# Kernel optimization log

Measured on AMD Instinct MI355X. Metric: run time of the kernel, lower is better.

## Reference

```python
import jax, jax.numpy as jnp
import numpy as np

WIN = 7      # window_size (square)
HEADS = 6    # num_heads


def setup_inputs() -> dict:
    key = jax.random.key(0)
    k0, k1, k2, k3 = jax.random.split(key, 4)
    B, C, H, W = 8, 384, 56, 56
    x = jax.random.normal(k0, (B, C, H, W), jnp.float32)
    # 1x1 conv weights stored as (out, in) matrices
    w_qkv = jax.random.normal(k1, (3 * C, C), jnp.float32) * 0.02
    b_qkv = jnp.zeros((3 * C,), jnp.float32)
    w_proj = jax.random.normal(k2, (C, C), jnp.float32) * 0.02
    b_proj = jnp.zeros((C,), jnp.float32)
    bias_table = jax.random.normal(k3, (WIN * WIN, HEADS), jnp.float32) * 0.02
    return {"x": x, "w_qkv": w_qkv, "b_qkv": b_qkv, "w_proj": w_proj,
            "b_proj": b_proj, "bias_table": bias_table}


def reference(x, w_qkv, b_qkv, w_proj, b_proj, bias_table):
    B, C, H, W = x.shape
    heads, win = HEADS, WIN
    dph = C // heads
    scale = dph ** -0.5
    # qkv 1x1 conv -> (B, 3C, H, W)
    qkv = jnp.einsum('bcij,oc->boij', x, w_qkv) + b_qkv[None, :, None, None]
    q = qkv[:, :C] * scale
    k = qkv[:, C:2 * C]
    v = qkv[:, 2 * C:]
    p = win // 2
    kp = jnp.pad(k, ((0, 0), (0, 0), (p, p), (p, p)))  # (B,C,H+6,W+6)
    vp = jnp.pad(v, ((0, 0), (0, 0), (p, p), (p, p)))
    qh = q.reshape(B, heads, dph, H, W)
    # local window QK scores: fixed 49 shifted slices (no big patch tensor)
    scores = []
    for idx in range(win * win):
        dy, dx = idx // win, idx % win
        ks = kp[:, :, dy:dy + H, dx:dx + W].reshape(B, heads, dph, H, W)
        scores.append(jnp.einsum('bhdij,bhdij->bhij', qh, ks))
    attn = jnp.stack(scores, axis=2)  # (B, heads, 49, H, W)
    # forward() adds relative_position_bias * 0 (faithful no-op)
    attn = attn + bias_table.T.reshape(1, heads, win * win, 1, 1) * 0.0
    attn = jax.nn.softmax(attn, axis=2)
    # apply attention to V via the same 49 shifted slices
    out = jnp.zeros((B, heads, dph, H, W), x.dtype)
    for idx in range(win * win):
        dy, dx = idx // win, idx % win
        vs = vp[:, :, dy:dy + H, dx:dx + W].reshape(B, heads, dph, H, W)
        out = out + attn[:, :, idx][:, :, None] * vs
    out = out.reshape(B, C, H, W)
    # proj 1x1 conv; proj_drop has p=0.0 -> identity
    out = jnp.einsum('bcij,oc->boij', out, w_proj) + b_proj[None, :, None, None]
    return out
```

## Files before the change

kernel.cpp:

```cpp
#include <hip/hip_runtime.h>
#include <hip/hip_bf16.h>
#include <stdint.h>

#define HWsz 3136
#define Hh   56
#define Cc   384
#define NHEADS 6
#define NB   8

typedef __attribute__((ext_vector_type(8))) short short8;
typedef __attribute__((ext_vector_type(4))) short short4v;
typedef __attribute__((ext_vector_type(4))) float f32x4;

static __device__ __forceinline__ short f2bf(float f) {
  __hip_bfloat16 h = __float2bfloat16(f);
  return (short)__builtin_bit_cast(unsigned short, h);
}

__global__ void prep_weights(const float* __restrict__ wq, const float* __restrict__ wp,
                             short* __restrict__ wqb, short* __restrict__ wpb) {
  int stride = gridDim.x * blockDim.x;
  for (int i = blockIdx.x * blockDim.x + threadIdx.x; i < 3 * Cc * Cc; i += stride) {
    float v = wq[i];
    if (i < Cc * Cc) v *= 0.125f;
    wqb[i] = f2bf(v);
  }
  for (int i = blockIdx.x * blockDim.x + threadIdx.x; i < Cc * Cc; i += stride)
    wpb[i] = f2bf(wp[i]);
}

__global__ __launch_bounds__(256) void transpose_x(const float* __restrict__ x, short* __restrict__ xT) {
  __shared__ float tile[32][33];
  int b = blockIdx.z;
  int p0 = blockIdx.x * 32, c0 = blockIdx.y * 32;
  int t = threadIdx.x;
  const float* xb = x + (size_t)b * Cc * HWsz;
  int tp = t & 31, tc = t >> 5;
#pragma unroll
  for (int cc = 0; cc < 4; ++cc)
    tile[tc + cc * 8][tp] = xb[(size_t)(c0 + tc + cc * 8) * HWsz + p0 + tp];
  __syncthreads();
  short* xo = xT + (size_t)b * HWsz * Cc;
  int wc = t & 31, wp = t >> 5;
#pragma unroll
  for (int pp = 0; pp < 4; ++pp)
    xo[(size_t)(p0 + wp + pp * 8) * Cc + c0 + wc] = f2bf(tile[wc][wp + pp * 8]);
}

template<int MODE>
__global__ __launch_bounds__(256) void gemm_bf16(
    const short* __restrict__ A, const short* __restrict__ Bm,
    const float* __restrict__ bias, void* __restrict__ o1, void* __restrict__ o2)
{
  constexpr int K = Cc;
  const int b   = blockIdx.z;
  const int om0 = blockIdx.x * 128;
  const int pn0 = blockIdx.y * 128;
  __shared__ short lA[128 * 40];
  __shared__ short lB[128 * 40];
  const int t    = threadIdx.x;
  const int lane = t & 63;
  const int wave = t >> 6;
  const int wm = (wave >> 1) * 64;
  const int wn = (wave & 1) * 64;
  f32x4 acc[4][4] = {};
  const short* Bb = Bm + (size_t)b * HWsz * K;
  const int sr = t >> 2;
  const int sk = (t & 3) * 8;
  int pr0 = pn0 + sr;      if (pr0 > HWsz - 1) pr0 = HWsz - 1;
  int pr1 = pn0 + sr + 64; if (pr1 > HWsz - 1) pr1 = HWsz - 1;
  const int fr = lane & 15;
  const int fo = lane >> 4;
  for (int k0 = 0; k0 < K; k0 += 32) {
    short8 a0 = *(const short8*)(A + (size_t)(om0 + sr) * K + k0 + sk);
    short8 a1 = *(const short8*)(A + (size_t)(om0 + sr + 64) * K + k0 + sk);
    short8 b0 = *(const short8*)(Bb + (size_t)pr0 * K + k0 + sk);
    short8 b1 = *(const short8*)(Bb + (size_t)pr1 * K + k0 + sk);
    __syncthreads();
    *(short8*)(lA + sr * 40 + sk) = a0;
    *(short8*)(lA + (sr + 64) * 40 + sk) = a1;
    *(short8*)(lB + sr * 40 + sk) = b0;
    *(short8*)(lB + (sr + 64) * 40 + sk) = b1;
    __syncthreads();
    short8 af[4], bfr[4];
#pragma unroll
    for (int m = 0; m < 4; ++m) af[m]  = *(const short8*)(lA + (wm + m * 16 + fr) * 40 + fo * 8);
#pragma unroll
    for (int n = 0; n < 4; ++n) bfr[n] = *(const short8*)(lB + (wn + n * 16 + fr) * 40 + fo * 8);
#pragma unroll
    for (int m = 0; m < 4; ++m)
#pragma unroll
      for (int n = 0; n < 4; ++n)
        acc[m][n] = __builtin_amdgcn_mfma_f32_16x16x32_bf16(af[m], bfr[n], acc[m][n], 0, 0, 0);
  }
  if (MODE == 0) {
    if (om0 < 768) {
      short* outq = (short*)o1 + (size_t)b * HWsz * 768;
#pragma unroll
      for (int m = 0; m < 4; ++m) {
        int ob = om0 + wm + m * 16 + (lane >> 4) * 4;
        float bs[4];
#pragma unroll
        for (int r = 0; r < 4; ++r) { int o = ob + r; bs[r] = bias[o] * (o < Cc ? 0.125f : 1.0f); }
#pragma unroll
        for (int n = 0; n < 4; ++n) {
          int p = pn0 + wn + n * 16 + fr;
          if (p < HWsz) {
            short4v s;
#pragma unroll
            for (int r = 0; r < 4; ++r) s[r] = f2bf(acc[m][n][r] + bs[r]);
            *(short4v*)(outq + (size_t)p * 768 + ob) = s;
          }
        }
      }
    } else {
      short* vtp = (short*)o2;
#pragma unroll
      for (int m = 0; m < 4; ++m) {
        int ob = om0 + wm + m * 16 + (lane >> 4) * 4;
#pragma unroll
        for (int n = 0; n < 4; ++n) {
          int p = pn0 + wn + n * 16 + fr;
          if (p < HWsz) {
            int ii = p / Hh, jj = p % Hh;
#pragma unroll
            for (int r = 0; r < 4; ++r) {
              int ch = ob + r - 768;
              vtp[((b * Cc + ch) * 62 + ii + 3) * 64 + jj + 3] = f2bf(acc[m][n][r] + bias[ob + r]);
            }
          }
        }
      }
    }
  } else {
    float* outo = (float*)o1 + (size_t)b * Cc * HWsz;
#pragma unroll
    for (int m = 0; m < 4; ++m) {
      int ob = om0 + wm + m * 16 + (lane >> 4) * 4;
#pragma unroll
      for (int n = 0; n < 4; ++n) {
        int p = pn0 + wn + n * 16 + fr;
        if (p < HWsz) {
#pragma unroll
          for (int r = 0; r < 4; ++r)
            outo[(size_t)(ob + r) * HWsz + p] = acc[m][n][r] + bias[ob + r];
        }
      }
    }
  }
}

__global__ __launch_bounds__(256) void attn_mfma(
    const short* __restrict__ qkv,
    const short* __restrict__ vtp,
    short* __restrict__ aout)
{
  __shared__ short P[64 * 40];
  const int bh = blockIdx.z;
  const int b = bh / NHEADS, h = bh % NHEADS;
  const int i0 = blockIdx.y * 8, j0 = blockIdx.x * 8;
  const int t = threadIdx.x, lane = t & 63, w = t >> 6;
  const int fr = lane & 15, fo = lane >> 4;

  const int q_idx = w * 16 + fr;
  const int qr = q_idx >> 3, qc = q_idx & 7;
  const int qkvb = b * HWsz * 768;

  const short* qp = qkv + qkvb + ((i0 + qr) * Hh + j0 + qc) * 768 + h * 64 + fo * 8;
  short8 qf0 = *(const short8*)(qp);
  short8 qf1 = *(const short8*)(qp + 32);

  const int kj = j0 + fr - 3;
  const bool jok = (unsigned)kj < (unsigned)Hh;
  const int kjs = kj < 0 ? 0 : (kj > Hh - 1 ? Hh - 1 : kj);
  const short* kcol = qkv + qkvb + Cc + h * 64 + fo * 8;

  const short8 z = (short8)0;
  f32x4 oacc[4] = {};
  float sum = 0.f;

#pragma unroll 2
  for (int kc = 0; kc < 7; ++kc) {
    short8 kf[2][2];
#pragma unroll
    for (int mloc = 0; mloc < 2; ++mloc) {
      int ki = i0 + 2 * kc + mloc - 3;
      bool ok = jok && ((unsigned)ki < (unsigned)Hh);
      int kis = ki < 0 ? 0 : (ki > Hh - 1 ? Hh - 1 : ki);
      const short8* ka = (const short8*)(kcol + (kis * Hh + kjs) * 768);
      short8 k0 = ka[0], k1 = ka[4];
      kf[mloc][0] = ok ? k0 : z;
      kf[mloc][1] = ok ? k1 : z;
    }
    short8 vf[4];
    const int vrow = i0 + 2 * kc + (fo >> 1);
    const int vcol = j0 + (fo & 1) * 8;
#pragma unroll
    for (int n = 0; n < 4; ++n)
      vf[n] = *(const short8*)(vtp + ((b * Cc + h * 64 + 16 * n + fr) * 62 + vrow) * 64 + vcol);
    f32x4 s0 = {}, s1 = {};
    s0 = __builtin_amdgcn_mfma_f32_16x16x32_bf16(kf[0][0], qf0, s0, 0, 0, 0);
    s0 = __builtin_amdgcn_mfma_f32_16x16x32_bf16(kf[0][1], qf1, s0, 0, 0, 0);
    s1 = __builtin_amdgcn_mfma_f32_16x16x32_bf16(kf[1][0], qf0, s1, 0, 0, 0);
    s1 = __builtin_amdgcn_mfma_f32_16x16x32_bf16(kf[1][1], qf1, s1, 0, 0, 0);
#pragma unroll
    for (int mloc = 0; mloc < 2; ++mloc) {
      const f32x4 sv = mloc ? s1 : s0;
      int dpr = 2 * kc + mloc - qr;
      bool rok = (unsigned)dpr <= 6u;
      short4v pk;
#pragma unroll
      for (int r = 0; r < 4; ++r) {
        int dpc = fo * 4 + r - qc;
        float e = (rok && (unsigned)dpc <= 6u) ? __expf(sv[r]) : 0.f;
        sum += e;
        pk[r] = f2bf(e);
      }
      *(short4v*)(P + q_idx * 40 + mloc * 16 + fo * 4) = pk;
    }
    short8 pa = *(const short8*)(P + q_idx * 40 + fo * 8);
#pragma unroll
    for (int n = 0; n < 4; ++n)
      oacc[n] = __builtin_amdgcn_mfma_f32_16x16x32_bf16(pa, vf[n], oacc[n], 0, 0, 0);
  }

  sum += __shfl_xor(sum, 16);
  sum += __shfl_xor(sum, 32);
  float inv[4];
#pragma unroll
  for (int r = 0; r < 4; ++r) inv[r] = 1.0f / __shfl(sum, fo * 4 + r);
  const int owr = i0 + 2 * w + (fo >> 1);
  const int owc = j0 + (fo & 1) * 4;
#pragma unroll
  for (int n = 0; n < 4; ++n)
#pragma unroll
    for (int r = 0; r < 4; ++r)
      aout[(size_t)(b * HWsz + owr * Hh + owc + r) * Cc + h * 64 + 16 * n + fr] =
          f2bf(oacc[n][r] * inv[r]);
}

extern "C" void kernel_launch(void* const* d_in, const int* in_sizes, int n_in,
                              void* d_out, int out_size, void* d_ws, size_t ws_size,
                              hipStream_t stream) {
  const float* x      = (const float*)d_in[0];
  const float* w_qkv  = (const float*)d_in[1];
  const float* b_qkv  = (const float*)d_in[2];
  const float* w_proj = (const float*)d_in[3];
  const float* b_proj = (const float*)d_in[4];

  char* ws = (char*)d_ws;
  short* qk  = (short*)ws;
  short* vtp = (short*)(ws + 38535168);
  short* xT  = (short*)(ws + 38535168 + 24379392);
  short* wqb = (short*)(ws + 38535168 + 24379392 + 19267584);
  short* wpb = (short*)(ws + 38535168 + 24379392 + 19267584 + 884736);

  prep_weights<<<512, 256, 0, stream>>>(w_qkv, w_proj, wqb, wpb);
  transpose_x<<<dim3(98, 12, NB), 256, 0, stream>>>(x, xT);
  hipMemsetAsync(vtp, 0, 24379392, stream);
  gemm_bf16<0><<<dim3(9, 25, NB), 256, 0, stream>>>(wqb, xT, b_qkv, qk, vtp);
  attn_mfma<<<dim3(7, 7, NB * NHEADS), 256, 0, stream>>>(qk, vtp, xT);
  gemm_bf16<1><<<dim3(3, 25, NB), 256, 0, stream>>>(wpb, xT, b_proj, d_out, nullptr);
}
```

Before: 256.4 us.

## Fuse x transpose and bf16 conversion into QKV GEMM loader; flatten grids

Removes the separate transpose_x kernel. The QKV GEMM now reads fp32 x directly in channel-major layout, converts pairs of channels to bf16 and writes them transposed into shared memory. Grids are also flattened to 1D with the batch index in the low bits, so neighbouring blocks come from different batches. This saves a kernel launch and a full write-plus-read of the bf16 xT buffer, at the cost of fp32 global loads and scattered 32-bit LDS stores inside the GEMM loop.

```diff
diff --git a/kernel.cpp b/kernel.cpp
--- a/kernel.cpp
+++ b/kernel.cpp
@@ -29,33 +29,17 @@
     wpb[i] = f2bf(wp[i]);
 }
 
-__global__ __launch_bounds__(256) void transpose_x(const float* __restrict__ x, short* __restrict__ xT) {
-  __shared__ float tile[32][33];
-  int b = blockIdx.z;
-  int p0 = blockIdx.x * 32, c0 = blockIdx.y * 32;
-  int t = threadIdx.x;
-  const float* xb = x + (size_t)b * Cc * HWsz;
-  int tp = t & 31, tc = t >> 5;
-#pragma unroll
-  for (int cc = 0; cc < 4; ++cc)
-    tile[tc + cc * 8][tp] = xb[(size_t)(c0 + tc + cc * 8) * HWsz + p0 + tp];
-  __syncthreads();
-  short* xo = xT + (size_t)b * HWsz * Cc;
-  int wc = t & 31, wp = t >> 5;
-#pragma unroll
-  for (int pp = 0; pp < 4; ++pp)
-    xo[(size_t)(p0 + wp + pp * 8) * Cc + c0 + wc] = f2bf(tile[wc][wp + pp * 8]);
-}
-
 template<int MODE>
 __global__ __launch_bounds__(256) void gemm_bf16(
-    const short* __restrict__ A, const short* __restrict__ Bm,
+    const short* __restrict__ A, const void* __restrict__ Bsrc,
     const float* __restrict__ bias, void* __restrict__ o1, void* __restrict__ o2)
 {
   constexpr int K = Cc;
-  const int b   = blockIdx.z;
-  const int om0 = blockIdx.x * 128;
-  const int pn0 = blockIdx.y * 128;
+  constexpr int NOM = (MODE == 0 ? 9 : 3);
+  const int b   = blockIdx.x & 7;
+  const int idx = blockIdx.x >> 3;
+  const int om0 = (idx % NOM) * 128;
+  const int pn0 = (idx / NOM) * 128;
   __shared__ short lA[128 * 40];
   __shared__ short lB[128 * 40];
   const int t    = threadIdx.x;
@@ -64,23 +48,50 @@
   const int wm = (wave >> 1) * 64;
   const int wn = (wave & 1) * 64;
   f32x4 acc[4][4] = {};
-  const short* Bb = Bm + (size_t)b * HWsz * K;
+  const int fr = lane & 15;
+  const int fo = lane >> 4;
   const int sr = t >> 2;
   const int sk = (t & 3) * 8;
+  const int pg = t & 15, cpair = t >> 4;
+  const int pbase = pn0 + pg * 8;
+  const int po0 = pbase     > HWsz - 4 ? HWsz - 4 : pbase;
+  const int po1 = pbase + 4 > HWsz - 4 ? HWsz - 4 : pbase + 4;
+  const float* Bx = (const float*)Bsrc + (size_t)b * Cc * HWsz;
+  const short* Bb = (const short*)Bsrc + (size_t)b * HWsz * K;
   int pr0 = pn0 + sr;      if (pr0 > HWsz - 1) pr0 = HWsz - 1;
   int pr1 = pn0 + sr + 64; if (pr1 > HWsz - 1) pr1 = HWsz - 1;
-  const int fr = lane & 15;
-  const int fo = lane >> 4;
+
   for (int k0 = 0; k0 < K; k0 += 32) {
     short8 a0 = *(const short8*)(A + (size_t)(om0 + sr) * K + k0 + sk);
     short8 a1 = *(const short8*)(A + (size_t)(om0 + sr + 64) * K + k0 + sk);
-    short8 b0 = *(const short8*)(Bb + (size_t)pr0 * K + k0 + sk);
-    short8 b1 = *(const short8*)(Bb + (size_t)pr1 * K + k0 + sk);
+    f32x4 x00, x01, x10, x11; short8 b0, b1;
+    if (MODE == 0) {
+      const float* r0 = Bx + (size_t)(k0 + 2 * cpair) * HWsz;
+      x00 = *(const f32x4*)(r0 + po0);
+      x01 = *(const f32x4*)(r0 + po1);
+      x10 = *(const f32x4*)(r0 + HWsz + po0);
+      x11 = *(const f32x4*)(r0 + HWsz + po1);
+    } else {
+      b0 = *(const short8*)(Bb + (size_t)pr0 * K + k0 + sk);
+      b1 = *(const short8*)(Bb + (size_t)pr1 * K + k0 + sk);
+    }
     __syncthreads();
     *(short8*)(lA + sr * 40 + sk) = a0;
     *(short8*)(lA + (sr + 64) * 40 + sk) = a1;
-    *(short8*)(lB + sr * 40 + sk) = b0;
-    *(short8*)(lB + (sr + 64) * 40 + sk) = b1;
+    if (MODE == 0) {
+      uint32_t* lB32 = (uint32_t*)lB;
+#pragma unroll
+      for (int qq = 0; qq < 8; ++qq) {
+        float va = (qq < 4) ? x00[qq] : x01[qq - 4];
+        float vb = (qq < 4) ? x10[qq] : x11[qq - 4];
+        uint32_t pk = (uint32_t)(unsigned short)f2bf(va) |
+                      ((uint32_t)(unsigned short)f2bf(vb) << 16);
+        lB32[((pg * 8 + qq) * 40 + 2 * cpair) >> 1] = pk;
+      }
+    } else {
+      *(short8*)(lB + sr * 40 + sk) = b0;
+      *(short8*)(lB + (sr + 64) * 40 + sk) = b1;
+    }
     __syncthreads();
     short8 af[4], bfr[4];
 #pragma unroll
@@ -156,9 +167,12 @@
     short* __restrict__ aout)
 {
   __shared__ short P[64 * 40];
-  const int bh = blockIdx.z;
-  const int b = bh / NHEADS, h = bh % NHEADS;
-  const int i0 = blockIdx.y * 8, j0 = blockIdx.x * 8;
+  const int blk = blockIdx.x;
+  const int b = blk & 7;
+  const int r_ = blk >> 3;
+  const int h = r_ / 49;
+  const int tile = r_ % 49;
+  const int i0 = (tile / 7) * 8, j0 = (tile % 7) * 8;
   const int t = threadIdx.x, lane = t & 63, w = t >> 6;
   const int fr = lane & 15, fo = lane >> 4;
 
@@ -249,16 +263,15 @@
   const float* b_proj = (const float*)d_in[4];
 
   char* ws = (char*)d_ws;
-  short* qk  = (short*)ws;
-  short* vtp = (short*)(ws + 38535168);
-  short* xT  = (short*)(ws + 38535168 + 24379392);
-  short* wqb = (short*)(ws + 38535168 + 24379392 + 19267584);
-  short* wpb = (short*)(ws + 38535168 + 24379392 + 19267584 + 884736);
+  short* qk   = (short*)ws;
+  short* vtp  = (short*)(ws + 38535168);
+  short* aout = (short*)(ws + 38535168 + 24379392);
+  short* wqb  = (short*)(ws + 38535168 + 24379392 + 19267584);
+  short* wpb  = (short*)(ws + 38535168 + 24379392 + 19267584 + 884736);
 
   prep_weights<<<512, 256, 0, stream>>>(w_qkv, w_proj, wqb, wpb);
-  transpose_x<<<dim3(98, 12, NB), 256, 0, stream>>>(x, xT);
   hipMemsetAsync(vtp, 0, 24379392, stream);
-  gemm_bf16<0><<<dim3(9, 25, NB), 256, 0, stream>>>(wqb, xT, b_qkv, qk, vtp);
-  attn_mfma<<<dim3(7, 7, NB * NHEADS), 256, 0, stream>>>(qk, vtp, xT);
-  gemm_bf16<1><<<dim3(3, 25, NB), 256, 0, stream>>>(wpb, xT, b_proj, d_out, nullptr);
-}
+  gemm_bf16<0><<<8 * 225, 256, 0, stream>>>(wqb, x, b_qkv, qk, vtp);
+  attn_mfma<<<8 * 294, 256, 0, stream>>>(qk, vtp, aout);
+  gemm_bf16<1><<<8 * 75, 256, 0, stream>>>(wpb, aout, b_proj, d_out, nullptr);
+}
```

Measured after the change: 261.0 us. Within noise of the previous version (+1.8%).

## Pre-tile GEMM operands into LDS-ready layout and load via global_load_lds

Applied to the files above, without the earlier changes.

Weights, transposed activations and the attention output are now written in a pre-tiled 128x40 padded block layout that matches the GEMM's shared-memory tiles. The GEMM then copies each k-slice straight from global to LDS with global_load_lds instead of staging through registers. Block indices are flattened with batch in the low bits to spread batches across CUs. This cuts GEMM load instructions and register pressure, at the cost of more complex producer kernels and scattered stores in the attention epilogue.

```diff
diff --git a/kernel.cpp b/kernel.cpp
--- a/kernel.cpp
+++ b/kernel.cpp
@@ -16,71 +16,96 @@
   __hip_bfloat16 h = __float2bfloat16(f);
   return (short)__builtin_bit_cast(unsigned short, h);
 }
+static __device__ __forceinline__ void gload16(const void* g, void* l) {
+  __builtin_amdgcn_global_load_lds(
+      (const __attribute__((address_space(1))) void*)g,
+      (__attribute__((address_space(3))) void*)l, 16, 0, 0);
+}
 
 __global__ void prep_weights(const float* __restrict__ wq, const float* __restrict__ wp,
-                             short* __restrict__ wqb, short* __restrict__ wpb) {
+                             short* __restrict__ wqt, short* __restrict__ wpt) {
   int stride = gridDim.x * blockDim.x;
   for (int i = blockIdx.x * blockDim.x + threadIdx.x; i < 3 * Cc * Cc; i += stride) {
-    float v = wq[i];
-    if (i < Cc * Cc) v *= 0.125f;
-    wqb[i] = f2bf(v);
-  }
-  for (int i = blockIdx.x * blockDim.x + threadIdx.x; i < Cc * Cc; i += stride)
-    wpb[i] = f2bf(wp[i]);
-}
-
-__global__ __launch_bounds__(256) void transpose_x(const float* __restrict__ x, short* __restrict__ xT) {
-  __shared__ float tile[32][33];
-  int b = blockIdx.z;
-  int p0 = blockIdx.x * 32, c0 = blockIdx.y * 32;
-  int t = threadIdx.x;
+    int o = i / Cc, k = i - o * Cc;
+    float v = wq[i] * (o < Cc ? 0.125f : 1.0f);
+    wqt[(((o >> 7) * 12 + (k >> 5)) * 128 + (o & 127)) * 40 + (k & 31)] = f2bf(v);
+  }
+  for (int i = blockIdx.x * blockDim.x + threadIdx.x; i < Cc * Cc; i += stride) {
+    int o = i / Cc, k = i - o * Cc;
+    wpt[(((o >> 7) * 12 + (k >> 5)) * 128 + (o & 127)) * 40 + (k & 31)] = f2bf(wp[i]);
+  }
+}
+
+__global__ __launch_bounds__(256) void transpose_x(const float* __restrict__ x,
+                                                   short* __restrict__ xTt) {
+  __shared__ float tf[32][129];
+  const int blk = blockIdx.x;
+  const int b = blk & 7;
+  const int idx = blk >> 3;
+  const int pni = idx >> 2;
+  const int kg  = idx & 3;
+  const int p0 = pni * 128;
+  const int t = threadIdx.x;
   const float* xb = x + (size_t)b * Cc * HWsz;
-  int tp = t & 31, tc = t >> 5;
-#pragma unroll
-  for (int cc = 0; cc < 4; ++cc)
-    tile[tc + cc * 8][tp] = xb[(size_t)(c0 + tc + cc * 8) * HWsz + p0 + tp];
-  __syncthreads();
-  short* xo = xT + (size_t)b * HWsz * Cc;
-  int wc = t & 31, wp = t >> 5;
-#pragma unroll
-  for (int pp = 0; pp < 4; ++pp)
-    xo[(size_t)(p0 + wp + pp * 8) * Cc + c0 + wc] = f2bf(tile[wc][wp + pp * 8]);
+  short* outb = xTt + ((size_t)(b * 25 + pni)) * 12 * 5120;
+  const int cc = t >> 3, pq = t & 7;
+  const int orow = t >> 1, ohf = t & 1;
+  for (int k0 = kg * 3; k0 < kg * 3 + 3; ++k0) {
+    const float* crow = xb + (size_t)(k0 * 32 + cc) * HWsz;
+#pragma unroll
+    for (int i = 0; i < 4; ++i) {
+      int p = p0 + pq * 16 + i * 4;
+      if (p > HWsz - 4) p = HWsz - 4;
+      f32x4 v = *(const f32x4*)(crow + p);
+      tf[cc][pq * 16 + i * 4 + 0] = v[0];
+      tf[cc][pq * 16 + i * 4 + 1] = v[1];
+      tf[cc][pq * 16 + i * 4 + 2] = v[2];
+      tf[cc][pq * 16 + i * 4 + 3] = v[3];
+    }
+    __syncthreads();
+    short8 s0, s1;
+#pragma unroll
+    for (int i = 0; i < 8; ++i) s0[i] = f2bf(tf[ohf * 16 + i][orow]);
+#pragma unroll
+    for (int i = 0; i < 8; ++i) s1[i] = f2bf(tf[ohf * 16 + 8 + i][orow]);
+    short* orp = outb + k0 * 5120 + orow * 40 + ohf * 16;
+    *(short8*)(orp)     = s0;
+    *(short8*)(orp + 8) = s1;
+    __syncthreads();
+  }
 }
 
 template<int MODE>
 __global__ __launch_bounds__(256) void gemm_bf16(
-    const short* __restrict__ A, const short* __restrict__ Bm,
+    const short* __restrict__ At, const short* __restrict__ Bt,
     const float* __restrict__ bias, void* __restrict__ o1, void* __restrict__ o2)
 {
-  constexpr int K = Cc;
-  const int b   = blockIdx.z;
-  const int om0 = blockIdx.x * 128;
-  const int pn0 = blockIdx.y * 128;
-  __shared__ short lA[128 * 40];
-  __shared__ short lB[128 * 40];
-  const int t    = threadIdx.x;
-  const int lane = t & 63;
-  const int wave = t >> 6;
-  const int wm = (wave >> 1) * 64;
-  const int wn = (wave & 1) * 64;
+  constexpr int NOM = (MODE == 0 ? 9 : 3);
+  const int b   = blockIdx.x & 7;
+  const int idx = blockIdx.x >> 3;
+  const int omi = idx % NOM;
+  const int pni = idx / NOM;
+  const int om0 = omi * 128, pn0 = pni * 128;
+  __shared__ short lA[5120];
+  __shared__ short lB[5120];
+  const int t = threadIdx.x, lane = t & 63, wave = t >> 6;
+  const int wm = (wave >> 1) * 64, wn = (wave & 1) * 64;
+  const int fr = lane & 15, fo = lane >> 4;
   f32x4 acc[4][4] = {};
-  const short* Bb = Bm + (size_t)b * HWsz * K;
-  const int sr = t >> 2;
-  const int sk = (t & 3) * 8;
-  int pr0 = pn0 + sr;      if (pr0 > HWsz - 1) pr0 = HWsz - 1;
-  int pr1 = pn0 + sr + 64; if (pr1 > HWsz - 1) pr1 = HWsz - 1;
-  const int fr = lane & 15;
-  const int fo = lane >> 4;
-  for (int k0 = 0; k0 < K; k0 += 32) {
-    short8 a0 = *(const short8*)(A + (size_t)(om0 + sr) * K + k0 + sk);
-    short8 a1 = *(const short8*)(A + (size_t)(om0 + sr + 64) * K + k0 + sk);
-    short8 b0 = *(const short8*)(Bb + (size_t)pr0 * K + k0 + sk);
-    short8 b1 = *(const short8*)(Bb + (size_t)pr1 * K + k0 + sk);
-    __syncthreads();
-    *(short8*)(lA + sr * 40 + sk) = a0;
-    *(short8*)(lA + (sr + 64) * 40 + sk) = a1;
-    *(short8*)(lB + sr * 40 + sk) = b0;
-    *(short8*)(lB + (sr + 64) * 40 + sk) = b1;
+  const short* Abase = At + omi * 12 * 5120;
+  const short* Bbase = Bt + ((size_t)(b * 25 + pni)) * 12 * 5120;
+
+  for (int k0i = 0; k0i < 12; ++k0i) {
+    __syncthreads();
+    const short* Ats = Abase + k0i * 5120;
+    const short* Bts = Bbase + k0i * 5120;
+#pragma unroll
+    for (int c = 0; c < 5; ++c) {
+      const int g = wave * 5 + c;
+      const short* src = (g < 10 ? Ats + g * 512 : Bts + (g - 10) * 512) + lane * 8;
+      short* dst = (g < 10 ? lA + g * 512 : lB + (g - 10) * 512);
+      gload16(src, dst);
+    }
     __syncthreads();
     short8 af[4], bfr[4];
 #pragma unroll
@@ -153,12 +178,15 @@
 __global__ __launch_bounds__(256) void attn_mfma(
     const short* __restrict__ qkv,
     const short* __restrict__ vtp,
-    short* __restrict__ aout)
+    short* __restrict__ aoutT)
 {
   __shared__ short P[64 * 40];
-  const int bh = blockIdx.z;
-  const int b = bh / NHEADS, h = bh % NHEADS;
-  const int i0 = blockIdx.y * 8, j0 = blockIdx.x * 8;
+  const int blk = blockIdx.x;
+  const int b = blk & 7;
+  const int r_ = blk >> 3;
+  const int h = r_ / 49;
+  const int tile = r_ % 49;
+  const int i0 = (tile / 7) * 8, j0 = (tile % 7) * 8;
   const int t = threadIdx.x, lane = t & 63, w = t >> 6;
   const int fr = lane & 15, fo = lane >> 4;
 
@@ -231,12 +259,17 @@
   for (int r = 0; r < 4; ++r) inv[r] = 1.0f / __shfl(sum, fo * 4 + r);
   const int owr = i0 + 2 * w + (fo >> 1);
   const int owc = j0 + (fo & 1) * 4;
-#pragma unroll
-  for (int n = 0; n < 4; ++n)
-#pragma unroll
-    for (int r = 0; r < 4; ++r)
-      aout[(size_t)(b * HWsz + owr * Hh + owc + r) * Cc + h * 64 + 16 * n + fr] =
-          f2bf(oacc[n][r] * inv[r]);
+  short* ab = aoutT + (size_t)b * 25 * 12 * 5120;
+#pragma unroll
+  for (int n = 0; n < 4; ++n) {
+    const int k0 = 2 * h + (n >> 1);
+    const int kk = 16 * (n & 1) + fr;
+#pragma unroll
+    for (int r = 0; r < 4; ++r) {
+      int p = owr * Hh + owc + r;
+      ab[((size_t)((p >> 7) * 12 + k0)) * 5120 + (p & 127) * 40 + kk] = f2bf(oacc[n][r] * inv[r]);
+    }
+  }
 }
 
 extern "C" void kernel_launch(void* const* d_in, const int* in_sizes, int n_in,
@@ -251,14 +284,14 @@
   char* ws = (char*)d_ws;
   short* qk  = (short*)ws;
   short* vtp = (short*)(ws + 38535168);
-  short* xT  = (short*)(ws + 38535168 + 24379392);
-  short* wqb = (short*)(ws + 38535168 + 24379392 + 19267584);
-  short* wpb = (short*)(ws + 38535168 + 24379392 + 19267584 + 884736);
-
-  prep_weights<<<512, 256, 0, stream>>>(w_qkv, w_proj, wqb, wpb);
-  transpose_x<<<dim3(98, 12, NB), 256, 0, stream>>>(x, xT);
+  short* xTt = (short*)(ws + 38535168 + 24379392);
+  short* wqt = (short*)(ws + 38535168 + 24379392 + 24576000);
+  short* wpt = (short*)(ws + 38535168 + 24379392 + 24576000 + 1105920);
+
+  prep_weights<<<512, 256, 0, stream>>>(w_qkv, w_proj, wqt, wpt);
   hipMemsetAsync(vtp, 0, 24379392, stream);
-  gemm_bf16<0><<<dim3(9, 25, NB), 256, 0, stream>>>(wqb, xT, b_qkv, qk, vtp);
-  attn_mfma<<<dim3(7, 7, NB * NHEADS), 256, 0, stream>>>(qk, vtp, xT);
-  gemm_bf16<1><<<dim3(3, 25, NB), 256, 0, stream>>>(wpb, xT, b_proj, d_out, nullptr);
-}
+  transpose_x<<<8 * 100, 256, 0, stream>>>(x, xTt);
+  gemm_bf16<0><<<8 * 225, 256, 0, stream>>>(wqt, xTt, b_qkv, qk, vtp);
+  attn_mfma<<<8 * 294, 256, 0, stream>>>(qk, vtp, xTt);
+  gemm_bf16<1><<<8 * 75, 256, 0, stream>>>(wpt, xTt, b_proj, d_out, nullptr);
+}
```

Result: faster. 236.8 us (-7.6%).
